# Performance work log

Hardware: AMD Instinct MI355X
Metric: run time of the kernel (lower is better)

The kernel has to match this reference:

```python
import jax, jax.numpy as jnp
import numpy as np

B, T, K = 512, 1024, 48
START, STOP, PAD = 45, 46, 47
NEG = -10000.0


def setup_inputs() -> dict:
    key = jax.random.key(0)
    k1, k2, k3 = jax.random.split(key, 3)
    h_tag = jax.random.normal(k1, (B, T, K), dtype=jnp.float32)
    # valid lengths in [T//2, T]; mask is float (used multiplicatively in the blend)
    lengths = jax.random.randint(k2, (B,), T // 2, T + 1)
    mask = (jnp.arange(T)[None, :] < lengths[:, None]).astype(jnp.float32)
    trans = jax.random.normal(k3, (K, K), dtype=jnp.float32)
    # replicate the CRF constraint initialization from the torch module
    trans = (trans.at[START, :].set(NEG)
                  .at[:, STOP].set(NEG)
                  .at[:, PAD].set(NEG)
                  .at[PAD, :].set(NEG)
                  .at[PAD, STOP].set(0.0)
                  .at[PAD, PAD].set(0.0))
    return {"h_tag": h_tag, "mask": mask, "trans": trans}


def _lse(x):
    # matches the module's log_sum_exp over the last axis
    m = jnp.max(x, axis=-1)
    return m + jnp.log(jnp.sum(jnp.exp(x - m[..., None]), axis=-1))


def reference(h_tag, mask, trans):
    Bsz, Tlen, Ktags = h_tag.shape
    score0 = jnp.full((Bsz, Ktags), NEG, dtype=h_tag.dtype).at[:, STOP].set(0.0)

    def step(score, xs):
        emit_t, mask_t = xs  # emit_t: [B, K], mask_t: [B]
        # score[b, j] + trans[i, j] + emit_t[b, i] -> [B, K(next=i), K(prev=j)]
        s = score[:, None, :] + trans[None, :, :] + emit_t[:, :, None]
        s = _lse(s)  # [B, K]
        m = mask_t[:, None]
        return s * m + score * (1.0 - m), None

    xs = (jnp.swapaxes(h_tag, 0, 1), mask.T)  # time-major for scan
    score, _ = jax.lax.scan(step, score0, xs)
    return _lse(score + trans[STOP])  # [B] log partition scores
```

## Files before the change

kernel.cpp:

```cpp
#include <hip/hip_runtime.h>
#include <hip/hip_bf16.h>

#define Bsz   512
#define Tlen  1024
#define Ktag  48
#define NREAL 45
#define HALF_T 512
#define STOPT 46
#define NEGV  -10000.0f
#define GB    16

typedef float          f32x4  __attribute__((ext_vector_type(4)));
typedef short          bf16x4 __attribute__((ext_vector_type(4)));
typedef unsigned short u16x4  __attribute__((ext_vector_type(4)));

#if defined(__has_builtin)
#  if __has_builtin(__builtin_amdgcn_mfma_f32_16x16x16bf16_1k)
#    define HAVE_MFMA16 1
#  endif
#endif
#ifndef HAVE_MFMA16
#  define HAVE_MFMA16 0
#endif


__device__ __forceinline__ float wave_max(float v) {
#pragma unroll
    for (int off = 32; off > 0; off >>= 1)
        v = fmaxf(v, __shfl_xor(v, off, 64));
    return v;
}
__device__ __forceinline__ float wave_sum(float v) {
#pragma unroll
    for (int off = 32; off > 0; off >>= 1)
        v += __shfl_xor(v, off, 64);
    return v;
}
__device__ __forceinline__ float bcast(float v, int l) {
    return __int_as_float(__builtin_amdgcn_readlane(__float_as_int(v), l));
}

template <bool BF16>
__device__ __forceinline__ float ld(const void* p, size_t i) {
    if constexpr (BF16) {
        unsigned int u = ((const unsigned short*)p)[i];
        return __uint_as_float(u << 16);
    } else {
        return ((const float*)p)[i];
    }
}

__device__ __forceinline__ unsigned pk2(float lo, float hi) {
    unsigned r;
    asm("v_cvt_pk_bf16_f32 %0, %1, %2" : "=v"(r) : "v"(lo), "v"(hi));
    return r;
}
__device__ __forceinline__ bf16x4 mk4(unsigned a, unsigned b) {
    union { unsigned u[2]; bf16x4 v; } c; c.u[0] = a; c.u[1] = b; return c.v;
}

template <bool BF16> struct EmT { using T = f32x4; };
template <>          struct EmT<true> { using T = u16x4; };

__device__ __forceinline__ f32x4 tof4(f32x4 v) { return v; }
__device__ __forceinline__ f32x4 tof4(u16x4 v) {
    f32x4 r;
    r.x = __uint_as_float((unsigned)v.x << 16);
    r.y = __uint_as_float((unsigned)v.y << 16);
    r.z = __uint_as_float((unsigned)v.z << 16);
    r.w = __uint_as_float((unsigned)v.w << 16);
    return r;
}

#if HAVE_MFMA16
__device__ __forceinline__ f32x4 mfma16(bf16x4 a, bf16x4 b, f32x4 c) {
    return __builtin_amdgcn_mfma_f32_16x16x16bf16_1k(a, b, c, 0, 0, 0);
}

__device__ __forceinline__ bf16x4 pk4(f32x4 u) {
    return mk4(pk2(u.x, u.y), pk2(u.z, u.w));
}
__device__ __forceinline__ bf16x4 pkmul(f32x4 u, f32x4 e) {
    return mk4(pk2(u.x * __expf(e.x), u.y * __expf(e.y)),
               pk2(u.z * __expf(e.z), u.w * __expf(e.w)));
}
__device__ __forceinline__ f32x4 mulexp(f32x4 a, f32x4 e) {
    f32x4 r;
    r.x = a.x * __expf(e.x); r.y = a.y * __expf(e.y);
    r.z = a.z * __expf(e.z); r.w = a.w * __expf(e.w);
    return r;
}
__device__ __forceinline__ f32x4 sel4(bool a, f32x4 x, f32x4 y) {
    f32x4 r;
    r.x = a ? x.x : y.x; r.y = a ? x.y : y.y;
    r.z = a ? x.z : y.z; r.w = a ? x.w : y.w;
    return r;
}

__device__ __forceinline__ int Ft1(int i, int k) { return ((3*i + 5*k) % 7) - 3; }
__device__ __forceinline__ int Gt1(int k, int c) { return ((2*k + 3*c) % 5) - 2; }
__device__ __forceinline__ int Ft2(int i, int k) { return ((5*i + 7*k) % 11) - 5; }
__device__ __forceinline__ int Gt2(int k, int c) { return ((3*k + 2*c) % 9) - 4; }

__device__ int probe_layout() {
    const int lane = threadIdx.x & 63;
    const int b = lane & 15, g = lane >> 4;
    float e1[4], e2[4];
#pragma unroll
    for (int r = 0; r < 4; r++) {
        int s1 = 0, s2 = 0;
        for (int k = 0; k < 16; k++) {
            s1 += Ft1(4*g + r, k) * Gt1(k, b);
            s2 += Ft2(4*g + r, k) * Gt2(k, b);
        }
        e1[r] = (float)s1; e2[r] = (float)s2;
    }
    int found = -1;
    for (int av = 0; av < 3; av++) {
        for (int bv = 0; bv < 3; bv++) {
            float A1[4], B1[4], A2[4], B2[4];
#pragma unroll
            for (int j = 0; j < 4; j++) {
                int ar, ak, bk, bc;
                if (av == 0)      { ar = b;       ak = 4*g + j; }
                else if (av == 1) { ar = b;       ak = g + 4*j; }
                else              { ar = 4*g + j; ak = b;       }
                if (bv == 0)      { bk = 4*g + j; bc = b;       }
                else if (bv == 1) { bk = g + 4*j; bc = b;       }
                else              { bk = b;       bc = 4*g + j; }
                A1[j] = (float)Ft1(ar, ak);  B1[j] = (float)Gt1(bk, bc);
                A2[j] = (float)Ft2(ar, ak);  B2[j] = (float)Gt2(bk, bc);
            }
            f32x4 z = {0.f, 0.f, 0.f, 0.f};
            f32x4 d1 = mfma16(mk4(pk2(A1[0],A1[1]), pk2(A1[2],A1[3])),
                              mk4(pk2(B1[0],B1[1]), pk2(B1[2],B1[3])), z);
            f32x4 d2 = mfma16(mk4(pk2(A2[0],A2[1]), pk2(A2[2],A2[3])),
                              mk4(pk2(B2[0],B2[1]), pk2(B2[2],B2[3])), z);
            bool ok = d1.x==e1[0] && d1.y==e1[1] && d1.z==e1[2] && d1.w==e1[3]
                   && d2.x==e2[0] && d2.y==e2[1] && d2.z==e2[2] && d2.w==e2[3];
            if (__all(ok) && found < 0) found = av*3 + bv;
        }
    }
    return found;
}

template <bool BF16>
__device__ void crf_mfma(const void* __restrict__ h, const void* __restrict__ mask,
                         const void* __restrict__ trans, float* __restrict__ ws,
                         int amap, float (*ltr)[Ktag + 1], float* lse) {
    using ET = typename EmT<BF16>::T;
    constexpr size_t esz = BF16 ? 2 : 4;

    const int lane = threadIdx.x;
    const int gw   = blockIdx.x;
    const bool fwd = gw < (Bsz / GB);
    const int b0   = (fwd ? gw : gw - (Bsz / GB)) * GB;
    const int b    = lane & 15;
    const int g    = lane >> 4;

    for (int idx = lane; idx < Ktag * Ktag; idx += 64)
        ltr[idx / Ktag][idx % Ktag] = ld<BF16>(trans, (size_t)idx);
    __syncthreads();

    if (fwd && lane < Ktag) {
        float mx = -3.0e38f;
        for (int j = 0; j < Ktag; j++)
            mx = fmaxf(mx, ltr[lane][j] + (j == STOPT ? 0.f : NEGV));
        float s = 0.f;
        for (int j = 0; j < Ktag; j++)
            s += __expf(ltr[lane][j] + (j == STOPT ? 0.f : NEGV) - mx);
        lse[lane] = mx + __logf(s);
    }
    __syncthreads();

    bf16x4 Eh[3][3], El[3][3];
#pragma unroll
    for (int m = 0; m < 3; m++) {
#pragma unroll
        for (int c = 0; c < 3; c++) {
            float x[4];
#pragma unroll
            for (int j = 0; j < 4; j++) {
                int rr, kk;
                if (amap == 0)      { rr = b;       kk = 4*g + j; }
                else if (amap == 1) { rr = b;       kk = g + 4*j; }
                else                { rr = 4*g + j; kk = b;       }
                int R = 16*m + rr, K = 16*c + kk;
                x[j] = fwd ? __expf(ltr[R][K]) : __expf(ltr[K][R]);
            }
            unsigned h01 = pk2(x[0], x[1]), h23 = pk2(x[2], x[3]);
            Eh[m][c] = mk4(h01, h23);
            float l0 = x[0] - __uint_as_float(h01 << 16);
            float l1 = x[1] - __uint_as_float(h01 & 0xFFFF0000u);
            float l2 = x[2] - __uint_as_float(h23 << 16);
            float l3 = x[3] - __uint_as_float(h23 & 0xFFFF0000u);
            El[m][c] = mk4(pk2(l0, l1), pk2(l2, l3));
        }
    }

    const char* hb = (const char*)h + ((size_t)(b0 + b) * Tlen * Ktag + 4 * g) * esz;

    float* uF = ws;
    float* MF = ws + (size_t)Bsz * Ktag;
    float* uB = MF + Bsz;
    float* MB = uB + (size_t)Bsz * Ktag;

    f32x4 U[3];
    float M;
    int lenv = 0;

    if (fwd) {
        f32x4 e0[3];
#pragma unroll
        for (int c = 0; c < 3; c++)
            e0[c] = tof4(*(const ET*)(hb + (size_t)(16 * c) * esz));
        float cmax = -3.0e38f;
        float sc[3][4];
#pragma unroll
        for (int c = 0; c < 3; c++)
#pragma unroll
            for (int j = 0; j < 4; j++) {
                int i = 16*c + 4*g + j;
                float v = (i < NREAL) ? (e0[c][j] + lse[i]) : -3.0e38f;
                sc[c][j] = v;
                cmax = fmaxf(cmax, v);
            }
        cmax = fmaxf(cmax, __shfl_xor(cmax, 16, 64));
        cmax = fmaxf(cmax, __shfl_xor(cmax, 32, 64));
        M = cmax;
#pragma unroll
        for (int c = 0; c < 3; c++)
#pragma unroll
            for (int j = 0; j < 4; j++)
                U[c][j] = (16*c + 4*g + j < NREAL) ? __expf(sc[c][j] - cmax) : 0.f;
    } else {
        const char* mb = (const char*)mask + (size_t)(b0 + b) * Tlen * esz;
        float cs = 0.f;
        for (int kk = 0; kk < Tlen / 16; kk++) {
            f32x4 v = tof4(*(const ET*)(mb + (size_t)(kk * 16 + 4 * g) * esz));
            cs += (v.x + v.y) + (v.z + v.w);
        }
        cs += __shfl_xor(cs, 16, 64);
        cs += __shfl_xor(cs, 32, 64);
        lenv = (int)(cs + 0.5f);

        float cmax = -3.0e38f;
        float gv[3][4];
#pragma unroll
        for (int c = 0; c < 3; c++)
#pragma unroll
            for (int j = 0; j < 4; j++) {
                gv[c][j] = ltr[STOPT][16*c + 4*g + j];
                cmax = fmaxf(cmax, gv[c][j]);
            }
        cmax = fmaxf(cmax, __shfl_xor(cmax, 16, 64));
        cmax = fmaxf(cmax, __shfl_xor(cmax, 32, 64));
        M = cmax;
#pragma unroll
        for (int c = 0; c < 3; c++)
#pragma unroll
            for (int j = 0; j < 4; j++)
                U[c][j] = __expf(gv[c][j] - cmax);
    }

    if (fwd) {
        ET em[4][3], emn[4][3];
#pragma unroll
        for (int k = 0; k < 4; k++)
#pragma unroll
            for (int c = 0; c < 3; c++)
                em[k][c] = *(const ET*)(hb + ((size_t)(1 + k) * Ktag + 16*c) * esz);
        for (int t = 1; t < HALF_T; t += 4) {
#pragma unroll
            for (int k = 0; k < 4; k++) {
                int tt = t + 4 + k; if (tt > HALF_T - 1) tt = HALF_T - 1;
#pragma unroll
                for (int c = 0; c < 3; c++)
                    emn[k][c] = *(const ET*)(hb + ((size_t)tt * Ktag + 16*c) * esz);
            }
#pragma unroll
            for (int k = 0; k < 4; k++) {
                if (t + k < HALF_T) {
                    bf16x4 V[3];
#pragma unroll
                    for (int c = 0; c < 3; c++) V[c] = pk4(U[c]);
                    f32x4 a0 = {0.f,0.f,0.f,0.f};
                    f32x4 a1 = {0.f,0.f,0.f,0.f};
                    f32x4 a2 = {0.f,0.f,0.f,0.f};
#pragma unroll
                    for (int c = 0; c < 3; c++) {
                        a0 = mfma16(Eh[0][c], V[c], a0);
                        a1 = mfma16(Eh[1][c], V[c], a1);
                        a2 = mfma16(Eh[2][c], V[c], a2);
                    }
#pragma unroll
                    for (int c = 0; c < 3; c++) {
                        a0 = mfma16(El[0][c], V[c], a0);
                        a1 = mfma16(El[1][c], V[c], a1);
                        a2 = mfma16(El[2][c], V[c], a2);
                    }
                    U[0] = mulexp(a0, tof4(em[k][0]));
                    U[1] = mulexp(a1, tof4(em[k][1]));
                    U[2] = mulexp(a2, tof4(em[k][2]));
                }
            }
            float mx = fmaxf(fmaxf(U[0].x, U[0].y), fmaxf(U[0].z, U[0].w));
            mx = fmaxf(mx, fmaxf(fmaxf(U[1].x, U[1].y), fmaxf(U[1].z, U[1].w)));
            mx = fmaxf(mx, fmaxf(fmaxf(U[2].x, U[2].y), fmaxf(U[2].z, U[2].w)));
            mx = fmaxf(mx, __shfl_xor(mx, 16, 64));
            mx = fmaxf(mx, __shfl_xor(mx, 32, 64));
            float inv = 1.0f / mx;
            U[0] *= inv; U[1] *= inv; U[2] *= inv;
            M += __logf(mx);
#pragma unroll
            for (int k = 0; k < 4; k++)
#pragma unroll
                for (int c = 0; c < 3; c++) em[k][c] = emn[k][c];
        }
#pragma unroll
        for (int c = 0; c < 3; c++)
#pragma unroll
            for (int j = 0; j < 4; j++)
                uF[(size_t)(b0 + b) * Ktag + 16*c + 4*g + j] = U[c][j];
        if (lane < GB) MF[b0 + lane] = M;
    } else {
        ET em[4][3], emn[4][3];
#pragma unroll
        for (int k = 0; k < 4; k++)
#pragma unroll
            for (int c = 0; c < 3; c++)
                em[k][c] = *(const ET*)(hb + ((size_t)(Tlen - 1 - k) * Ktag + 16*c) * esz);
        for (int tg = Tlen - 1; tg >= HALF_T; tg -= 4) {
#pragma unroll
            for (int k = 0; k < 4; k++) {
                int tt = tg - 4 - k; if (tt < HALF_T) tt = HALF_T;
#pragma unroll
                for (int c = 0; c < 3; c++)
                    emn[k][c] = *(const ET*)(hb + ((size_t)tt * Ktag + 16*c) * esz);
            }
#pragma unroll
            for (int k = 0; k < 4; k++) {
                const int t = tg - k;
                const bool act = (t < lenv);
                bf16x4 V[3];
#pragma unroll
                for (int c = 0; c < 3; c++) V[c] = pkmul(U[c], tof4(em[k][c]));
                f32x4 a0 = {0.f,0.f,0.f,0.f};
                f32x4 a1 = {0.f,0.f,0.f,0.f};
                f32x4 a2 = {0.f,0.f,0.f,0.f};
#pragma unroll
                for (int c = 0; c < 3; c++) {
                    a0 = mfma16(Eh[0][c], V[c], a0);
                    a1 = mfma16(Eh[1][c], V[c], a1);
                    a2 = mfma16(Eh[2][c], V[c], a2);
                }
#pragma unroll
                for (int c = 0; c < 3; c++) {
                    a0 = mfma16(El[0][c], V[c], a0);
                    a1 = mfma16(El[1][c], V[c], a1);
                    a2 = mfma16(El[2][c], V[c], a2);
                }
                U[0] = sel4(act, a0, U[0]);
                U[1] = sel4(act, a1, U[1]);
                U[2] = sel4(act, a2, U[2]);
            }
            float mx = fmaxf(fmaxf(U[0].x, U[0].y), fmaxf(U[0].z, U[0].w));
            mx = fmaxf(mx, fmaxf(fmaxf(U[1].x, U[1].y), fmaxf(U[1].z, U[1].w)));
            mx = fmaxf(mx, fmaxf(fmaxf(U[2].x, U[2].y), fmaxf(U[2].z, U[2].w)));
            mx = fmaxf(mx, __shfl_xor(mx, 16, 64));
            mx = fmaxf(mx, __shfl_xor(mx, 32, 64));
            float inv = 1.0f / mx;
            U[0] *= inv; U[1] *= inv; U[2] *= inv;
            M += __logf(mx);
#pragma unroll
            for (int k = 0; k < 4; k++)
#pragma unroll
                for (int c = 0; c < 3; c++) em[k][c] = emn[k][c];
        }
#pragma unroll
        for (int c = 0; c < 3; c++)
#pragma unroll
            for (int j = 0; j < 4; j++)
                uB[(size_t)(b0 + b) * Ktag + 16*c + 4*g + j] = U[c][j];
        if (lane < GB) MB[b0 + lane] = M;
    }
}
#endif

template <bool BF16>
__device__ void crf_valu(const void* __restrict__ h, const void* __restrict__ mask,
                         const void* __restrict__ trans, float* __restrict__ ws,
                         float (*ltr)[Ktag + 1]) {
    const int lane = threadIdx.x;
    const int bid  = blockIdx.x;
    const bool fwd = bid < Bsz;
    const int b    = fwd ? bid : bid - Bsz;

    for (int idx = lane; idx < Ktag * Ktag; idx += 64) {
        int i = idx / Ktag;
        ltr[i][idx - i * Ktag] = ld<BF16>(trans, (size_t)idx);
    }
    __syncthreads();

    float E[Ktag];
#pragma unroll
    for (int j = 0; j < Ktag; j++) E[j] = 0.f;
    if (lane < Ktag) {
        if (fwd) {
#pragma unroll
            for (int j = 0; j < Ktag; j++) E[j] = __expf(ltr[lane][j]);
        } else {
#pragma unroll
            for (int i = 0; i < Ktag; i++) E[i] = __expf(ltr[i][lane]);
        }
    }

    const int li = (lane < Ktag) ? lane : (Ktag - 1);
    const size_t hb = (size_t)b * Tlen * Ktag;

    float* uF = ws;
    float* MF = ws + (size_t)Bsz * Ktag;
    float* uB = MF + Bsz;
    float* MB = uB + (size_t)Bsz * Ktag;

    float u = 0.f, M = 0.f;

    if (fwd) {
        {
            float e0 = ld<BF16>(h, hb + li);
            float mx = -3.0e38f;
#pragma unroll
            for (int j = 0; j < Ktag; j++) {
                float v = ltr[li][j] + (j == STOPT ? 0.f : NEGV);
                mx = fmaxf(mx, v);
            }
            float s = 0.f;
#pragma unroll
            for (int j = 0; j < Ktag; j++) {
                float v = ltr[li][j] + (j == STOPT ? 0.f : NEGV);
                s += __expf(v - mx);
            }
            float sc = e0 + mx + __logf(s);
            if (lane >= NREAL) sc = -3.0e38f;
            float m1 = wave_max(sc);
            M = m1;
            u = (lane < NREAL) ? __expf(sc - m1) : 0.f;
        }
        float em[4], emn[4];
#pragma unroll
        for (int k = 0; k < 4; k++) {
            int tt = 1 + k; if (tt > HALF_T - 1) tt = HALF_T - 1;
            em[k] = ld<BF16>(h, hb + (size_t)tt * Ktag + li);
        }
        for (int t = 1; t < HALF_T; t += 4) {
#pragma unroll
            for (int k = 0; k < 4; k++) {
                int tt = t + 4 + k; if (tt > HALF_T - 1) tt = HALF_T - 1;
                emn[k] = ld<BF16>(h, hb + (size_t)tt * Ktag + li);
            }
#pragma unroll
            for (int k = 0; k < 4; k++) {
                if (t + k < HALF_T) {
                    float ee = __expf(em[k]);
                    float a0 = 0.f, a1 = 0.f, a2 = 0.f, a3 = 0.f;
#pragma unroll
                    for (int j = 0; j < Ktag; j += 4) {
                        a0 = fmaf(E[j + 0], bcast(u, j + 0), a0);
                        a1 = fmaf(E[j + 1], bcast(u, j + 1), a1);
                        a2 = fmaf(E[j + 2], bcast(u, j + 2), a2);
                        a3 = fmaf(E[j + 3], bcast(u, j + 3), a3);
                    }
                    u = ((a0 + a1) + (a2 + a3)) * ee;
                }
            }
            float m = wave_max(u);
            u *= 1.0f / m;
            M += __logf(m);
#pragma unroll
            for (int k = 0; k < 4; k++) em[k] = emn[k];
        }
        if (lane < Ktag) uF[(size_t)b * Ktag + lane] = u;
        if (lane == 0) MF[b] = M;
    } else {
        float c = 0.f;
        for (int t0 = lane; t0 < Tlen; t0 += 64)
            c += ld<BF16>(mask, (size_t)b * Tlen + t0);
        c = wave_sum(c);
        int len = (int)(c + 0.5f);

        float g = (lane < Ktag) ? ltr[STOPT][lane] : -3.0e38f;
        float m0 = wave_max(g);
        M = m0;
        u = (lane < Ktag) ? __expf(g - m0) : 0.f;

        int t0 = len - 1;
        float em[4], emn[4];
#pragma unroll
        for (int k = 0; k < 4; k++) {
            int tt = t0 - k; if (tt < HALF_T) tt = HALF_T;
            em[k] = ld<BF16>(h, hb + (size_t)tt * Ktag + li);
        }
        for (int tg = t0; tg >= HALF_T; tg -= 4) {
#pragma unroll
            for (int k = 0; k < 4; k++) {
                int tt = tg - 4 - k; if (tt < HALF_T) tt = HALF_T;
                emn[k] = ld<BF16>(h, hb + (size_t)tt * Ktag + li);
            }
#pragma unroll
            for (int k = 0; k < 4; k++) {
                if (tg - k >= HALF_T) {
                    float ee = __expf(em[k]);
                    float v = u * ee;
                    float a0 = 0.f, a1 = 0.f, a2 = 0.f, a3 = 0.f;
#pragma unroll
                    for (int j = 0; j < Ktag; j += 4) {
                        a0 = fmaf(E[j + 0], bcast(v, j + 0), a0);
                        a1 = fmaf(E[j + 1], bcast(v, j + 1), a1);
                        a2 = fmaf(E[j + 2], bcast(v, j + 2), a2);
                        a3 = fmaf(E[j + 3], bcast(v, j + 3), a3);
                    }
                    u = (a0 + a1) + (a2 + a3);
                }
            }
            float m = wave_max(u);
            u *= 1.0f / m;
            M += __logf(m);
#pragma unroll
            for (int k = 0; k < 4; k++) em[k] = emn[k];
        }
        if (lane < Ktag) uB[(size_t)b * Ktag + lane] = u;
        if (lane == 0) MB[b] = M;
    }
}

__global__ void __launch_bounds__(64) crf_main(const void* __restrict__ h,
                                               const void* __restrict__ mask,
                                               const void* __restrict__ trans,
                                               float* __restrict__ ws) {
    __shared__ float ltr_s[Ktag][Ktag + 1];
#if HAVE_MFMA16
    __shared__ float lse_s[Ktag];
#endif
    bool isbf16 = (((const unsigned short*)mask)[0] == 0x3F80);
#if HAVE_MFMA16
    int lay = probe_layout();
    if (lay >= 0 && (lay % 3) == 0) {
        if (blockIdx.x >= (2 * Bsz) / GB) return;
        int amap = lay / 3;
        if (isbf16) crf_mfma<true >(h, mask, trans, ws, amap, ltr_s, lse_s);
        else        crf_mfma<false>(h, mask, trans, ws, amap, ltr_s, lse_s);
        return;
    }
#endif
    if (isbf16) crf_valu<true >(h, mask, trans, ws, ltr_s);
    else        crf_valu<false>(h, mask, trans, ws, ltr_s);
}

__global__ void __launch_bounds__(64) crf_combine(const void* __restrict__ mask,
                                                  const float* __restrict__ ws,
                                                  void* __restrict__ out) {
    const int b = blockIdx.x;
    const int lane = threadIdx.x;
    const float* uF = ws;
    const float* MF = ws + (size_t)Bsz * Ktag;
    const float* uB = MF + Bsz;
    const float* MB = uB + (size_t)Bsz * Ktag;

    float p = (lane < Ktag) ? uF[(size_t)b * Ktag + lane] * uB[(size_t)b * Ktag + lane] : 0.f;
    float s = wave_sum(p);
    float ans = MF[b] + MB[b] + __logf(s);

    bool isbf16 = (((const unsigned short*)mask)[0] == 0x3F80);
    if (lane == 0) {
        if (isbf16) {
            unsigned int x = __float_as_uint(ans);
            unsigned int r = (x + 0x7FFFu + ((x >> 16) & 1u)) >> 16;
            ((unsigned short*)out)[b] = (unsigned short)r;
        } else {
            ((float*)out)[b] = ans;
        }
    }
}

extern "C" void kernel_launch(void* const* d_in, const int* in_sizes, int n_in,
                              void* d_out, int out_size, void* d_ws, size_t ws_size,
                              hipStream_t stream) {
    const void* h     = d_in[0];
    const void* mask  = d_in[1];
    const void* trans = d_in[2];
    float* ws = (float*)d_ws;

    hipLaunchKernelGGL(crf_main, dim3(2 * Bsz), dim3(64), 0, stream, h, mask, trans, ws);
    hipLaunchKernelGGL(crf_combine, dim3(Bsz), dim3(64), 0, stream, mask, ws, d_out);
}
```

Before: 262.2 us.

## Switch CRF recurrence to 16x16x32 bf16 MFMA with shuffled B operand

Replaces the 16x16x16 bf16 MFMA path with the wider 16x16x32 bf16 instruction. The 48-wide tag dimension is split into two K-tiles of 32 (zero-padded), and the state vector is rearranged into the B operand with lane shuffles. This cuts the MFMA count per step from 18 to 12 on the serial recurrence. In exchange it adds 12 shuffles and selects per step, a runtime layout probe plus feed check, and a fallback path that deliberately spins for a time that encodes which probe failed.

```diff
diff --git a/kernel.cpp b/kernel.cpp
--- a/kernel.cpp
+++ b/kernel.cpp
@@ -11,16 +11,16 @@
 #define GB    16
 
 typedef float          f32x4  __attribute__((ext_vector_type(4)));
-typedef short          bf16x4 __attribute__((ext_vector_type(4)));
+typedef short          bf16x8 __attribute__((ext_vector_type(8)));
 typedef unsigned short u16x4  __attribute__((ext_vector_type(4)));
 
 #if defined(__has_builtin)
-#  if __has_builtin(__builtin_amdgcn_mfma_f32_16x16x16bf16_1k)
-#    define HAVE_MFMA16 1
+#  if __has_builtin(__builtin_amdgcn_mfma_f32_16x16x32_bf16)
+#    define HAVE_MFMA32 1
 #  endif
 #endif
-#ifndef HAVE_MFMA16
-#  define HAVE_MFMA16 0
+#ifndef HAVE_MFMA32
+#  define HAVE_MFMA32 0
 #endif
 
 
@@ -54,9 +54,6 @@
     unsigned r;
     asm("v_cvt_pk_bf16_f32 %0, %1, %2" : "=v"(r) : "v"(lo), "v"(hi));
     return r;
-}
-__device__ __forceinline__ bf16x4 mk4(unsigned a, unsigned b) {
-    union { unsigned u[2]; bf16x4 v; } c; c.u[0] = a; c.u[1] = b; return c.v;
 }
 
 template <bool BF16> struct EmT { using T = f32x4; };
@@ -72,18 +69,29 @@
     return r;
 }
 
-#if HAVE_MFMA16
-__device__ __forceinline__ f32x4 mfma16(bf16x4 a, bf16x4 b, f32x4 c) {
-    return __builtin_amdgcn_mfma_f32_16x16x16bf16_1k(a, b, c, 0, 0, 0);
-}
-
-__device__ __forceinline__ bf16x4 pk4(f32x4 u) {
-    return mk4(pk2(u.x, u.y), pk2(u.z, u.w));
-}
-__device__ __forceinline__ bf16x4 pkmul(f32x4 u, f32x4 e) {
-    return mk4(pk2(u.x * __expf(e.x), u.y * __expf(e.y)),
-               pk2(u.z * __expf(e.z), u.w * __expf(e.w)));
-}
+__device__ void spin_us(unsigned us) {
+#if defined(__has_builtin)
+#if __has_builtin(__builtin_amdgcn_s_memrealtime) && __has_builtin(__builtin_amdgcn_s_sleep)
+    unsigned long long t0 = __builtin_amdgcn_s_memrealtime();
+    unsigned long long tgt = (unsigned long long)us * 100ull;
+    while (__builtin_amdgcn_s_memrealtime() - t0 < tgt)
+        __builtin_amdgcn_s_sleep(8);
+#endif
+#endif
+}
+
+#if HAVE_MFMA32
+__device__ __forceinline__ f32x4 mfma32(bf16x8 a, bf16x8 b, f32x4 c) {
+    return __builtin_amdgcn_mfma_f32_16x16x32_bf16(a, b, c, 0, 0, 0);
+}
+
+__device__ __forceinline__ bf16x8 pack8(const float x[8]) {
+    union { unsigned u[4]; bf16x8 v; } c;
+    c.u[0] = pk2(x[0], x[1]); c.u[1] = pk2(x[2], x[3]);
+    c.u[2] = pk2(x[4], x[5]); c.u[3] = pk2(x[6], x[7]);
+    return c.v;
+}
+
 __device__ __forceinline__ f32x4 mulexp(f32x4 a, f32x4 e) {
     f32x4 r;
     r.x = a.x * __expf(e.x); r.y = a.y * __expf(e.y);
@@ -97,19 +105,58 @@
     return r;
 }
 
+__device__ __forceinline__ int amap_k(int av, int g, int j) {
+    return (av == 0) ? (8*g + j)
+         : (av == 1) ? (g + 4*j)
+         :             (4*g + (j & 3) + 16*(j >> 2));
+}
+
+__device__ __forceinline__ void step_core(const bf16x8 Eh[3][2], const bf16x8 El[3][2],
+                                          const unsigned Wm[3][2], int g, int b,
+                                          f32x4 acc[3]) {
+    const int l0 = ((g & 1) << 5) + b;
+    const int l1 = l0 + 16;
+    unsigned y00 = (unsigned)__shfl((int)Wm[0][0], l0, 64);
+    unsigned y01 = (unsigned)__shfl((int)Wm[0][1], l0, 64);
+    unsigned y02 = (unsigned)__shfl((int)Wm[0][0], l1, 64);
+    unsigned y03 = (unsigned)__shfl((int)Wm[0][1], l1, 64);
+    unsigned y10 = (unsigned)__shfl((int)Wm[1][0], l0, 64);
+    unsigned y11 = (unsigned)__shfl((int)Wm[1][1], l0, 64);
+    unsigned y12 = (unsigned)__shfl((int)Wm[1][0], l1, 64);
+    unsigned y13 = (unsigned)__shfl((int)Wm[1][1], l1, 64);
+    unsigned z0  = (unsigned)__shfl((int)Wm[2][0], l0, 64);
+    unsigned z1  = (unsigned)__shfl((int)Wm[2][1], l0, 64);
+    unsigned z2  = (unsigned)__shfl((int)Wm[2][0], l1, 64);
+    unsigned z3  = (unsigned)__shfl((int)Wm[2][1], l1, 64);
+    const bool hm = (g >= 2);
+    union { unsigned u[4]; bf16x8 v; } B0c, B1c;
+    B0c.u[0] = hm ? y10 : y00;  B0c.u[1] = hm ? y11 : y01;
+    B0c.u[2] = hm ? y12 : y02;  B0c.u[3] = hm ? y13 : y03;
+    B1c.u[0] = hm ? 0u : z0;    B1c.u[1] = hm ? 0u : z1;
+    B1c.u[2] = hm ? 0u : z2;    B1c.u[3] = hm ? 0u : z3;
+    bf16x8 Bk0 = B0c.v, Bk1 = B1c.v;
+#pragma unroll
+    for (int m = 0; m < 3; m++) {
+        acc[m] = mfma32(Eh[m][0], Bk0, acc[m]);
+        acc[m] = mfma32(Eh[m][1], Bk1, acc[m]);
+        acc[m] = mfma32(El[m][0], Bk0, acc[m]);
+        acc[m] = mfma32(El[m][1], Bk1, acc[m]);
+    }
+}
+
 __device__ __forceinline__ int Ft1(int i, int k) { return ((3*i + 5*k) % 7) - 3; }
 __device__ __forceinline__ int Gt1(int k, int c) { return ((2*k + 3*c) % 5) - 2; }
 __device__ __forceinline__ int Ft2(int i, int k) { return ((5*i + 7*k) % 11) - 5; }
 __device__ __forceinline__ int Gt2(int k, int c) { return ((3*k + 2*c) % 9) - 4; }
 
-__device__ int probe_layout() {
+__device__ int probe32() {
     const int lane = threadIdx.x & 63;
     const int b = lane & 15, g = lane >> 4;
     float e1[4], e2[4];
 #pragma unroll
     for (int r = 0; r < 4; r++) {
         int s1 = 0, s2 = 0;
-        for (int k = 0; k < 16; k++) {
+        for (int k = 0; k < 32; k++) {
             s1 += Ft1(4*g + r, k) * Gt1(k, b);
             s2 += Ft2(4*g + r, k) * Gt2(k, b);
         }
@@ -117,31 +164,70 @@
     }
     int found = -1;
     for (int av = 0; av < 3; av++) {
-        for (int bv = 0; bv < 3; bv++) {
-            float A1[4], B1[4], A2[4], B2[4];
-#pragma unroll
-            for (int j = 0; j < 4; j++) {
-                int ar, ak, bk, bc;
-                if (av == 0)      { ar = b;       ak = 4*g + j; }
-                else if (av == 1) { ar = b;       ak = g + 4*j; }
-                else              { ar = 4*g + j; ak = b;       }
-                if (bv == 0)      { bk = 4*g + j; bc = b;       }
-                else if (bv == 1) { bk = g + 4*j; bc = b;       }
-                else              { bk = b;       bc = 4*g + j; }
-                A1[j] = (float)Ft1(ar, ak);  B1[j] = (float)Gt1(bk, bc);
-                A2[j] = (float)Ft2(ar, ak);  B2[j] = (float)Gt2(bk, bc);
+        for (int bv = 0; bv < 4; bv++) {
+            float A1[8], B1[8], A2[8], B2[8];
+#pragma unroll
+            for (int j = 0; j < 8; j++) {
+                int ak = amap_k(av, g, j);
+                int bk, bc;
+                if (bv < 3) { bk = amap_k(bv, g, j); bc = b; }
+                else        { bk = b + 16*(j >> 2);  bc = 4*g + (j & 3); }
+                A1[j] = (float)Ft1(b, ak);  B1[j] = (float)Gt1(bk, bc);
+                A2[j] = (float)Ft2(b, ak);  B2[j] = (float)Gt2(bk, bc);
             }
             f32x4 z = {0.f, 0.f, 0.f, 0.f};
-            f32x4 d1 = mfma16(mk4(pk2(A1[0],A1[1]), pk2(A1[2],A1[3])),
-                              mk4(pk2(B1[0],B1[1]), pk2(B1[2],B1[3])), z);
-            f32x4 d2 = mfma16(mk4(pk2(A2[0],A2[1]), pk2(A2[2],A2[3])),
-                              mk4(pk2(B2[0],B2[1]), pk2(B2[2],B2[3])), z);
+            f32x4 d1 = mfma32(pack8(A1), pack8(B1), z);
+            f32x4 d2 = mfma32(pack8(A2), pack8(B2), z);
             bool ok = d1.x==e1[0] && d1.y==e1[1] && d1.z==e1[2] && d1.w==e1[3]
                    && d2.x==e2[0] && d2.y==e2[1] && d2.z==e2[2] && d2.w==e2[3];
-            if (__all(ok) && found < 0) found = av*3 + bv;
+            if (__all(ok) && found < 0) found = av*4 + bv;
         }
     }
     return found;
+}
+
+__device__ __forceinline__ int uvali(int r, int c) { return ((5*r + 3*c) % 9) - 4; }
+__device__ __forceinline__ int f3i(int i, int kg)  { return (kg < 48) ? (((2*i + kg) % 7) - 3) : 0; }
+
+__device__ bool feed_check(int amap) {
+    const int lane = threadIdx.x & 63;
+    const int b = lane & 15, g = lane >> 4;
+    bf16x8 Eh[3][2], El[3][2];
+#pragma unroll
+    for (int m = 0; m < 3; m++)
+#pragma unroll
+        for (int kt = 0; kt < 2; kt++) {
+            float x[8], zz[8];
+#pragma unroll
+            for (int j = 0; j < 8; j++) {
+                int kg = 32*kt + amap_k(amap, g, j);
+                x[j]  = (float)f3i(16*m + b, kg);
+                zz[j] = 0.f;
+            }
+            Eh[m][kt] = pack8(x); El[m][kt] = pack8(zz);
+        }
+    unsigned Wm[3][2];
+    f32x4 U[3];
+#pragma unroll
+    for (int m = 0; m < 3; m++) {
+#pragma unroll
+        for (int r = 0; r < 4; r++) U[m][r] = (float)uvali(16*m + 4*g + r, b);
+        Wm[m][0] = pk2(U[m].x, U[m].y);
+        Wm[m][1] = pk2(U[m].z, U[m].w);
+    }
+    f32x4 acc[3] = {{0,0,0,0},{0,0,0,0},{0,0,0,0}};
+    step_core(Eh, El, Wm, g, b, acc);
+    bool ok = true;
+#pragma unroll
+    for (int m = 0; m < 3; m++)
+#pragma unroll
+        for (int r = 0; r < 4; r++) {
+            int e = 0;
+            for (int kg = 0; kg < 48; kg++)
+                e += f3i(16*m + 4*g + r, kg) * uvali(kg, b);
+            ok = ok && (acc[m][r] == (float)e);
+        }
+    return __all(ok) != 0;
 }
 
 template <bool BF16>
@@ -173,30 +259,26 @@
     }
     __syncthreads();
 
-    bf16x4 Eh[3][3], El[3][3];
-#pragma unroll
-    for (int m = 0; m < 3; m++) {
-#pragma unroll
-        for (int c = 0; c < 3; c++) {
-            float x[4];
-#pragma unroll
-            for (int j = 0; j < 4; j++) {
-                int rr, kk;
-                if (amap == 0)      { rr = b;       kk = 4*g + j; }
-                else if (amap == 1) { rr = b;       kk = g + 4*j; }
-                else                { rr = 4*g + j; kk = b;       }
-                int R = 16*m + rr, K = 16*c + kk;
-                x[j] = fwd ? __expf(ltr[R][K]) : __expf(ltr[K][R]);
-            }
-            unsigned h01 = pk2(x[0], x[1]), h23 = pk2(x[2], x[3]);
-            Eh[m][c] = mk4(h01, h23);
-            float l0 = x[0] - __uint_as_float(h01 << 16);
-            float l1 = x[1] - __uint_as_float(h01 & 0xFFFF0000u);
-            float l2 = x[2] - __uint_as_float(h23 << 16);
-            float l3 = x[3] - __uint_as_float(h23 & 0xFFFF0000u);
-            El[m][c] = mk4(pk2(l0, l1), pk2(l2, l3));
-        }
-    }
+    bf16x8 Eh[3][2], El[3][2];
+#pragma unroll
+    for (int m = 0; m < 3; m++)
+#pragma unroll
+        for (int kt = 0; kt < 2; kt++) {
+            float x[8], lo[8];
+#pragma unroll
+            for (int j = 0; j < 8; j++) {
+                int kg = 32*kt + amap_k(amap, g, j);
+                float v = 0.f;
+                if (kg < 48)
+                    v = fwd ? __expf(ltr[16*m + b][kg]) : __expf(ltr[kg][16*m + b]);
+                x[j] = v;
+                unsigned u = __float_as_uint(v);
+                unsigned hb = ((u + 0x7FFFu + ((u >> 16) & 1u)) >> 16) << 16;
+                lo[j] = v - __uint_as_float(hb);
+            }
+            Eh[m][kt] = pack8(x);
+            El[m][kt] = pack8(lo);
+        }
 
     const char* hb = (const char*)h + ((size_t)(b0 + b) * Tlen * Ktag + 4 * g) * esz;
 
@@ -281,27 +363,17 @@
 #pragma unroll
             for (int k = 0; k < 4; k++) {
                 if (t + k < HALF_T) {
-                    bf16x4 V[3];
-#pragma unroll
-                    for (int c = 0; c < 3; c++) V[c] = pk4(U[c]);
-                    f32x4 a0 = {0.f,0.f,0.f,0.f};
-                    f32x4 a1 = {0.f,0.f,0.f,0.f};
-                    f32x4 a2 = {0.f,0.f,0.f,0.f};
-#pragma unroll
-                    for (int c = 0; c < 3; c++) {
-                        a0 = mfma16(Eh[0][c], V[c], a0);
-                        a1 = mfma16(Eh[1][c], V[c], a1);
-                        a2 = mfma16(Eh[2][c], V[c], a2);
+                    unsigned Wm[3][2];
+#pragma unroll
+                    for (int m = 0; m < 3; m++) {
+                        Wm[m][0] = pk2(U[m].x, U[m].y);
+                        Wm[m][1] = pk2(U[m].z, U[m].w);
                     }
-#pragma unroll
-                    for (int c = 0; c < 3; c++) {
-                        a0 = mfma16(El[0][c], V[c], a0);
-                        a1 = mfma16(El[1][c], V[c], a1);
-                        a2 = mfma16(El[2][c], V[c], a2);
-                    }
-                    U[0] = mulexp(a0, tof4(em[k][0]));
-                    U[1] = mulexp(a1, tof4(em[k][1]));
-                    U[2] = mulexp(a2, tof4(em[k][2]));
+                    f32x4 acc[3] = {{0,0,0,0},{0,0,0,0},{0,0,0,0}};
+                    step_core(Eh, El, Wm, g, b, acc);
+                    U[0] = mulexp(acc[0], tof4(em[k][0]));
+                    U[1] = mulexp(acc[1], tof4(em[k][1]));
+                    U[2] = mulexp(acc[2], tof4(em[k][2]));
                 }
             }
             float mx = fmaxf(fmaxf(U[0].x, U[0].y), fmaxf(U[0].z, U[0].w));
@@ -342,27 +414,18 @@
             for (int k = 0; k < 4; k++) {
                 const int t = tg - k;
                 const bool act = (t < lenv);
-                bf16x4 V[3];
-#pragma unroll
-                for (int c = 0; c < 3; c++) V[c] = pkmul(U[c], tof4(em[k][c]));
-                f32x4 a0 = {0.f,0.f,0.f,0.f};
-                f32x4 a1 = {0.f,0.f,0.f,0.f};
-                f32x4 a2 = {0.f,0.f,0.f,0.f};
-#pragma unroll
-                for (int c = 0; c < 3; c++) {
-                    a0 = mfma16(Eh[0][c], V[c], a0);
-                    a1 = mfma16(Eh[1][c], V[c], a1);
-                    a2 = mfma16(Eh[2][c], V[c], a2);
+                unsigned Wm[3][2];
+#pragma unroll
+                for (int m = 0; m < 3; m++) {
+                    f32x4 e = tof4(em[k][m]);
+                    Wm[m][0] = pk2(U[m].x * __expf(e.x), U[m].y * __expf(e.y));
+                    Wm[m][1] = pk2(U[m].z * __expf(e.z), U[m].w * __expf(e.w));
                 }
-#pragma unroll
-                for (int c = 0; c < 3; c++) {
-                    a0 = mfma16(El[0][c], V[c], a0);
-                    a1 = mfma16(El[1][c], V[c], a1);
-                    a2 = mfma16(El[2][c], V[c], a2);
-                }
-                U[0] = sel4(act, a0, U[0]);
-                U[1] = sel4(act, a1, U[1]);
-                U[2] = sel4(act, a2, U[2]);
+                f32x4 acc[3] = {{0,0,0,0},{0,0,0,0},{0,0,0,0}};
+                step_core(Eh, El, Wm, g, b, acc);
+                U[0] = sel4(act, acc[0], U[0]);
+                U[1] = sel4(act, acc[1], U[1]);
+                U[2] = sel4(act, acc[2], U[2]);
             }
             float mx = fmaxf(fmaxf(U[0].x, U[0].y), fmaxf(U[0].z, U[0].w));
             mx = fmaxf(mx, fmaxf(fmaxf(U[1].x, U[1].y), fmaxf(U[1].z, U[1].w)));
@@ -538,22 +601,32 @@
                                                const void* __restrict__ trans,
                                                float* __restrict__ ws) {
     __shared__ float ltr_s[Ktag][Ktag + 1];
-#if HAVE_MFMA16
+#if HAVE_MFMA32
     __shared__ float lse_s[Ktag];
 #endif
     bool isbf16 = (((const unsigned short*)mask)[0] == 0x3F80);
-#if HAVE_MFMA16
-    int lay = probe_layout();
-    if (lay >= 0 && (lay % 3) == 0) {
+#if HAVE_MFMA32
+    int lay = probe32();
+    bool ok = false;
+    int amap = 0;
+    if (lay >= 0 && (lay & 3) == 0) {
+        amap = lay >> 2;
+        ok = feed_check(amap);
+    }
+    if (ok) {
         if (blockIdx.x >= (2 * Bsz) / GB) return;
-        int amap = lay / 3;
         if (isbf16) crf_mfma<true >(h, mask, trans, ws, amap, ltr_s, lse_s);
         else        crf_mfma<false>(h, mask, trans, ws, amap, ltr_s, lse_s);
         return;
     }
-#endif
+    int code = (lay < 0) ? 0 : (((lay & 3) == 0) ? 13 : lay + 1);
     if (isbf16) crf_valu<true >(h, mask, trans, ws, ltr_s);
     else        crf_valu<false>(h, mask, trans, ws, ltr_s);
+    if (blockIdx.x == 0 && threadIdx.x == 0) spin_us(30 + 40 * (unsigned)code);
+#else
+    if (isbf16) crf_valu<true >(h, mask, trans, ws, ltr_s);
+    else        crf_valu<false>(h, mask, trans, ws, ltr_s);
+#endif
 }
 
 __global__ void __launch_bounds__(64) crf_combine(const void* __restrict__ mask,
```

After: 447.1 us. +70.5%, slower.
